# Kernel optimization log

Measured on AMD Instinct MI355X. Metric: run time of the kernel, lower is better.

The kernel has to match this reference:

```python
import jax, jax.numpy as jnp
import numpy as np

DIM = 32  # fixed internal node dim
N_GRAPHS = 64


def setup_inputs() -> dict:
    key = jax.random.key(0)
    ks = jax.random.split(key, 16)
    N, E, F_N, F_E, H = 12500, 200000, 16, 8, 32
    inp = {
        "x": jax.random.normal(ks[0], (N, F_N), dtype=jnp.float32),
        "edge_index": jax.random.randint(ks[1], (2, E), 0, N, dtype=jnp.int64),
        "edge_attr": jax.random.normal(ks[2], (E, F_E), dtype=jnp.float32),
        "batch": jnp.sort(jax.random.randint(ks[3], (N,), 0, N_GRAPHS, dtype=jnp.int64)),
        "lin0_w": jax.random.normal(ks[4], (DIM, F_N), dtype=jnp.float32) * 0.1,
        "lin0_b": jax.random.normal(ks[5], (DIM,), dtype=jnp.float32) * 0.1,
        "nn_w": jax.random.normal(ks[6], (DIM * H, F_E), dtype=jnp.float32) * 0.1,
        "nn_b": jax.random.normal(ks[7], (DIM * H,), dtype=jnp.float32) * 0.1,
        "root_w": jax.random.normal(ks[8], (DIM, H), dtype=jnp.float32) * 0.1,
        "conv_b": jax.random.normal(ks[9], (H,), dtype=jnp.float32) * 0.1,
        "lin1_w": jax.random.normal(ks[10], (16, H), dtype=jnp.float32) * 0.1,
        "lin1_b": jax.random.normal(ks[11], (16,), dtype=jnp.float32) * 0.1,
        "lin2_w": jax.random.normal(ks[12], (1, 16), dtype=jnp.float32) * 0.1,
        "lin2_b": jax.random.normal(ks[13], (1,), dtype=jnp.float32) * 0.1,
    }
    return inp


def reference(x, edge_index, edge_attr, batch, lin0_w, lin0_b, nn_w, nn_b,
              root_w, conv_b, lin1_w, lin1_b, lin2_w, lin2_b):
    N = x.shape[0]
    H = conv_b.shape[0]
    # lin0 + relu -> node features [N, DIM]
    out = jax.nn.relu(x @ lin0_w.T + lin0_b)
    # NNConv: per-edge weight matrices from edge MLP (single Linear)
    src, dst = edge_index[0], edge_index[1]
    w_e = (edge_attr @ nn_w.T + nn_b).reshape(-1, DIM, H)  # [E, DIM, H]
    msg = jnp.einsum('ed,edh->eh', out[src], w_e)          # gather + per-edge matmul
    agg = jax.ops.segment_sum(msg, dst, num_segments=N)     # scatter-add
    h = jax.nn.relu(agg + out @ root_w + conv_b)             # root weight + bias
    # global add pool over graphs
    u = jax.ops.segment_sum(h, batch, num_segments=N_GRAPHS)  # [G, H]
    o = jax.nn.relu(u @ lin1_w.T + lin1_b)
    o = o @ lin2_w.T + lin2_b
    return o.reshape(-1)
```

## Files before the change

kernel.cpp:

```cpp
#include <hip/hip_runtime.h>

#define DIMN 32
#define HD   32
#define FN   16
#define FE   8
#define NG   64

__global__ __launch_bounds__(256) void k1_node_pre(
    const float* __restrict__ x, const float* __restrict__ lin0_w,
    const float* __restrict__ lin0_b, const float* __restrict__ nn_w,
    const float* __restrict__ nn_b,
    float* __restrict__ outn, float* __restrict__ G, float* __restrict__ bmsg,
    int N, int nodes_per_block)
{
    __shared__ float s_nnw[DIMN * HD * FE];
    __shared__ float s_nnb[DIMN * HD];
    __shared__ float s_l0w[DIMN * FN];
    __shared__ float s_l0b[DIMN];
    __shared__ float s_out[DIMN];

    const int tid = threadIdx.x;
    for (int i = tid; i < DIMN * HD * FE; i += 256) s_nnw[i] = nn_w[i];
    for (int i = tid; i < DIMN * HD; i += 256)      s_nnb[i] = nn_b[i];
    for (int i = tid; i < DIMN * FN; i += 256)      s_l0w[i] = lin0_w[i];
    if (tid < DIMN) s_l0b[tid] = lin0_b[tid];
    __syncthreads();

    const int n0 = blockIdx.x * nodes_per_block;
    const int n1 = min(n0 + nodes_per_block, N);
    for (int n = n0; n < n1; ++n) {
        if (tid < DIMN) {
            float s = s_l0b[tid];
            const float* xr = x + (size_t)n * FN;
            #pragma unroll
            for (int j = 0; j < FN; ++j) s = fmaf(xr[j], s_l0w[tid * FN + j], s);
            s = fmaxf(s, 0.f);
            s_out[tid] = s;
            outn[(size_t)n * DIMN + tid] = s;
        }
        __syncthreads();

        float g = 0.f;
        #pragma unroll 8
        for (int d = 0; d < DIMN; ++d)
            g = fmaf(s_out[d], s_nnw[d * 256 + tid], g);
        G[(size_t)n * 256 + tid] = g;

        if (tid < HD) {
            float b = 0.f;
            #pragma unroll 8
            for (int d = 0; d < DIMN; ++d)
                b = fmaf(s_out[d], s_nnb[d * HD + tid], b);
            bmsg[(size_t)n * HD + tid] = b;
        }
        __syncthreads();
    }
}

__global__ __launch_bounds__(256) void k2_edge(
    const int* __restrict__ ei, const float* __restrict__ ea,
    const float* __restrict__ G, const float* __restrict__ bmsg,
    float* __restrict__ agg, int E)
{
    const int t = blockIdx.x * 256 + threadIdx.x;
    const int e = t >> 5;
    const int h = t & 31;
    if (e >= E) return;

    const int src = ei[e];
    const int dst = ei[E + e];

    const float* gp = G + (size_t)src * 256 + h * 8;
    const float4 ga = *(const float4*)(gp);
    const float4 gb = *(const float4*)(gp + 4);
    const float4 e0 = *(const float4*)(ea + (size_t)e * 8);
    const float4 e1 = *(const float4*)(ea + (size_t)e * 8 + 4);

    float acc = bmsg[(size_t)src * HD + h];
    acc = fmaf(e0.x, ga.x, acc);
    acc = fmaf(e0.y, ga.y, acc);
    acc = fmaf(e0.z, ga.z, acc);
    acc = fmaf(e0.w, ga.w, acc);
    acc = fmaf(e1.x, gb.x, acc);
    acc = fmaf(e1.y, gb.y, acc);
    acc = fmaf(e1.z, gb.z, acc);
    acc = fmaf(e1.w, gb.w, acc);

    atomicAdd(agg + (size_t)dst * HD + h, acc);
}

__global__ __launch_bounds__(256) void k3_node_upd(
    const float* __restrict__ agg, const float* __restrict__ outn,
    const float* __restrict__ root_w, const float* __restrict__ conv_b,
    const int* __restrict__ batch, float* __restrict__ u, int N)
{
    __shared__ float s_rw[DIMN * HD];
    __shared__ float s_cb[HD];
    const int tid = threadIdx.x;
    for (int i = tid; i < DIMN * HD; i += 256) s_rw[i] = root_w[i];
    if (tid < HD) s_cb[tid] = conv_b[tid];
    __syncthreads();

    const int t = blockIdx.x * 256 + tid;
    const int n = t >> 5;
    const int h = t & 31;
    if (n >= N) return;

    float v = agg[(size_t)n * HD + h] + s_cb[h];
    const float* orow = outn + (size_t)n * DIMN;
    #pragma unroll 8
    for (int k = 0; k < DIMN; ++k)
        v = fmaf(orow[k], s_rw[k * HD + h], v);
    v = fmaxf(v, 0.f);

    atomicAdd(u + (size_t)batch[n] * HD + h, v);
}

__global__ __launch_bounds__(64) void k4_head(
    const float* __restrict__ u, const float* __restrict__ lin1_w,
    const float* __restrict__ lin1_b, const float* __restrict__ lin2_w,
    const float* __restrict__ lin2_b, float* __restrict__ outp)
{
    const int g = threadIdx.x;
    if (g >= NG) return;

    float ur[HD];
    #pragma unroll
    for (int hh = 0; hh < HD; ++hh) ur[hh] = u[(size_t)g * HD + hh];

    float acc = lin2_b[0];
    #pragma unroll
    for (int i = 0; i < 16; ++i) {
        float o = lin1_b[i];
        #pragma unroll
        for (int hh = 0; hh < HD; ++hh)
            o = fmaf(ur[hh], lin1_w[i * HD + hh], o);
        o = fmaxf(o, 0.f);
        acc = fmaf(o, lin2_w[i], acc);
    }
    outp[g] = acc;
}

extern "C" void kernel_launch(void* const* d_in, const int* in_sizes, int n_in,
                              void* d_out, int out_size, void* d_ws, size_t ws_size,
                              hipStream_t stream)
{
    const float* x      = (const float*)d_in[0];
    const int*   ei     = (const int*)  d_in[1];
    const float* ea     = (const float*)d_in[2];
    const int*   batch  = (const int*)  d_in[3];
    const float* lin0_w = (const float*)d_in[4];
    const float* lin0_b = (const float*)d_in[5];
    const float* nn_w   = (const float*)d_in[6];
    const float* nn_b   = (const float*)d_in[7];
    const float* root_w = (const float*)d_in[8];
    const float* conv_b = (const float*)d_in[9];
    const float* lin1_w = (const float*)d_in[10];
    const float* lin1_b = (const float*)d_in[11];
    const float* lin2_w = (const float*)d_in[12];
    const float* lin2_b = (const float*)d_in[13];

    const int N = in_sizes[0] / FN;
    const int E = in_sizes[2] / FE;

    float* ws   = (float*)d_ws;
    float* outn = ws;
    float* G    = outn + (size_t)N * DIMN;
    float* bmsg = G    + (size_t)N * 256;
    float* agg  = bmsg + (size_t)N * DIMN;
    float* u    = agg  + (size_t)N * DIMN;

    hipMemsetAsync(agg, 0, (size_t)N * DIMN * sizeof(float), stream);
    hipMemsetAsync(u,   0, (size_t)NG * HD * sizeof(float), stream);

    const int npb = 16;
    const int nb1 = (N + npb - 1) / npb;
    k1_node_pre<<<nb1, 256, 0, stream>>>(x, lin0_w, lin0_b, nn_w, nn_b,
                                         outn, G, bmsg, N, npb);

    const int nb2 = (E * 32 + 255) / 256;
    k2_edge<<<nb2, 256, 0, stream>>>(ei, ea, G, bmsg, agg, E);

    const int nb3 = (N * 32 + 255) / 256;
    k3_node_upd<<<nb3, 256, 0, stream>>>(agg, outn, root_w, conv_b, batch, u, N);

    k4_head<<<1, 64, 0, stream>>>(u, lin1_w, lin1_b, lin2_w, lin2_b, (float*)d_out);
}
```

Measured before the change: 173.8 us.

## Replace atomic edge scatter with CSR-by-destination gather and segmented pooling

Builds a destination-sorted edge list each call (histogram, scan, scatter) and computes each node's aggregated message by pulling its incoming edges, fusing the root update and ReLU. Global pooling is replaced by a per-graph binary-search segment reduction fused with the MLP head. This removes millions of float atomics and the memsets. In exchange it adds three extra launches, a serial single-block scan, dependent indirect loads and load imbalance across nodes with varying in-degree.

```diff
diff --git a/kernel.cpp b/kernel.cpp
--- a/kernel.cpp
+++ b/kernel.cpp
@@ -11,6 +11,7 @@
     const float* __restrict__ lin0_b, const float* __restrict__ nn_w,
     const float* __restrict__ nn_b,
     float* __restrict__ outn, float* __restrict__ G, float* __restrict__ bmsg,
+    int* __restrict__ cnt,
     int N, int nodes_per_block)
 {
     __shared__ float s_nnw[DIMN * HD * FE];
@@ -20,6 +21,9 @@
     __shared__ float s_out[DIMN];
 
     const int tid = threadIdx.x;
+    const int gz = blockIdx.x * 256 + tid;
+    if (gz < N) cnt[gz] = 0;
+
     for (int i = tid; i < DIMN * HD * FE; i += 256) s_nnw[i] = nn_w[i];
     for (int i = tid; i < DIMN * HD; i += 256)      s_nnb[i] = nn_b[i];
     for (int i = tid; i < DIMN * FN; i += 256)      s_l0w[i] = lin0_w[i];
@@ -57,42 +61,56 @@
     }
 }
 
-__global__ __launch_bounds__(256) void k2_edge(
+__global__ __launch_bounds__(256) void k_hist(
+    const int* __restrict__ ei, int* __restrict__ cnt, int E)
+{
+    const int e = blockIdx.x * 256 + threadIdx.x;
+    if (e < E) atomicAdd(&cnt[ei[E + e]], 1);
+}
+
+__global__ __launch_bounds__(256) void k_scan(
+    const int* __restrict__ cnt, int* __restrict__ offs, int* __restrict__ cur, int N)
+{
+    __shared__ int s[256];
+    const int tid = threadIdx.x;
+    const int C = (N + 255) / 256;
+    const int lo = tid * C, hi = min(lo + C, N);
+    int sum = 0;
+    for (int i = lo; i < hi; ++i) sum += cnt[i];
+    s[tid] = sum;
+    __syncthreads();
+    for (int off = 1; off < 256; off <<= 1) {
+        int v = (tid >= off) ? s[tid - off] : 0;
+        __syncthreads();
+        s[tid] += v;
+        __syncthreads();
+    }
+    int run = (tid == 0) ? 0 : s[tid - 1];
+    for (int i = lo; i < hi; ++i) {
+        offs[i] = run;
+        cur[i]  = run;
+        run += cnt[i];
+    }
+    if (tid == 0) offs[N] = s[255];
+}
+
+__global__ __launch_bounds__(256) void k_scatter(
+    const int* __restrict__ ei, int* __restrict__ cur, int* __restrict__ eids, int E)
+{
+    const int e = blockIdx.x * 256 + threadIdx.x;
+    if (e < E) {
+        int p = atomicAdd(&cur[ei[E + e]], 1);
+        eids[p] = e;
+    }
+}
+
+__global__ __launch_bounds__(256) void k2_gather(
     const int* __restrict__ ei, const float* __restrict__ ea,
     const float* __restrict__ G, const float* __restrict__ bmsg,
-    float* __restrict__ agg, int E)
-{
-    const int t = blockIdx.x * 256 + threadIdx.x;
-    const int e = t >> 5;
-    const int h = t & 31;
-    if (e >= E) return;
-
-    const int src = ei[e];
-    const int dst = ei[E + e];
-
-    const float* gp = G + (size_t)src * 256 + h * 8;
-    const float4 ga = *(const float4*)(gp);
-    const float4 gb = *(const float4*)(gp + 4);
-    const float4 e0 = *(const float4*)(ea + (size_t)e * 8);
-    const float4 e1 = *(const float4*)(ea + (size_t)e * 8 + 4);
-
-    float acc = bmsg[(size_t)src * HD + h];
-    acc = fmaf(e0.x, ga.x, acc);
-    acc = fmaf(e0.y, ga.y, acc);
-    acc = fmaf(e0.z, ga.z, acc);
-    acc = fmaf(e0.w, ga.w, acc);
-    acc = fmaf(e1.x, gb.x, acc);
-    acc = fmaf(e1.y, gb.y, acc);
-    acc = fmaf(e1.z, gb.z, acc);
-    acc = fmaf(e1.w, gb.w, acc);
-
-    atomicAdd(agg + (size_t)dst * HD + h, acc);
-}
-
-__global__ __launch_bounds__(256) void k3_node_upd(
-    const float* __restrict__ agg, const float* __restrict__ outn,
-    const float* __restrict__ root_w, const float* __restrict__ conv_b,
-    const int* __restrict__ batch, float* __restrict__ u, int N)
+    const float* __restrict__ outn, const float* __restrict__ root_w,
+    const float* __restrict__ conv_b,
+    const int* __restrict__ offs, const int* __restrict__ eids,
+    float* __restrict__ hout, int N, int E)
 {
     __shared__ float s_rw[DIMN * HD];
     __shared__ float s_cb[HD];
@@ -106,39 +124,77 @@
     const int h = t & 31;
     if (n >= N) return;
 
-    float v = agg[(size_t)n * HD + h] + s_cb[h];
+    float acc = 0.f;
+    const int lo = offs[n], hi = offs[n + 1];
+    for (int j = lo; j < hi; ++j) {
+        const int e   = eids[j];
+        const int src = ei[e];
+        const float* gp = G + (size_t)src * 256 + h * 8;
+        const float4 ga = *(const float4*)(gp);
+        const float4 gb = *(const float4*)(gp + 4);
+        const float4 e0 = *(const float4*)(ea + (size_t)e * 8);
+        const float4 e1 = *(const float4*)(ea + (size_t)e * 8 + 4);
+        float m = bmsg[(size_t)src * HD + h];
+        m = fmaf(e0.x, ga.x, m);
+        m = fmaf(e0.y, ga.y, m);
+        m = fmaf(e0.z, ga.z, m);
+        m = fmaf(e0.w, ga.w, m);
+        m = fmaf(e1.x, gb.x, m);
+        m = fmaf(e1.y, gb.y, m);
+        m = fmaf(e1.z, gb.z, m);
+        m = fmaf(e1.w, gb.w, m);
+        acc += m;
+    }
+
+    float v = acc + s_cb[h];
     const float* orow = outn + (size_t)n * DIMN;
     #pragma unroll 8
     for (int k = 0; k < DIMN; ++k)
         v = fmaf(orow[k], s_rw[k * HD + h], v);
-    v = fmaxf(v, 0.f);
-
-    atomicAdd(u + (size_t)batch[n] * HD + h, v);
-}
-
-__global__ __launch_bounds__(64) void k4_head(
-    const float* __restrict__ u, const float* __restrict__ lin1_w,
-    const float* __restrict__ lin1_b, const float* __restrict__ lin2_w,
-    const float* __restrict__ lin2_b, float* __restrict__ outp)
-{
-    const int g = threadIdx.x;
-    if (g >= NG) return;
-
-    float ur[HD];
-    #pragma unroll
-    for (int hh = 0; hh < HD; ++hh) ur[hh] = u[(size_t)g * HD + hh];
-
-    float acc = lin2_b[0];
-    #pragma unroll
-    for (int i = 0; i < 16; ++i) {
-        float o = lin1_b[i];
+    hout[(size_t)n * HD + h] = fmaxf(v, 0.f);
+}
+
+__global__ __launch_bounds__(64) void k4_pool_head(
+    const float* __restrict__ hout, const int* __restrict__ batch,
+    const float* __restrict__ lin1_w, const float* __restrict__ lin1_b,
+    const float* __restrict__ lin2_w, const float* __restrict__ lin2_b,
+    float* __restrict__ outp, int N)
+{
+    const int g = blockIdx.x;
+    const int tid = threadIdx.x;
+
+    int a = 0, b = N;
+    while (a < b) { int m = (a + b) >> 1; if (batch[m] < g) a = m + 1; else b = m; }
+    const int lo = a;
+    b = N;
+    while (a < b) { int m = (a + b) >> 1; if (batch[m] < g + 1) a = m + 1; else b = m; }
+    const int hi = a;
+
+    __shared__ float s_u[HD];
+    __shared__ float s_o[16];
+
+    const int h = tid & 31, half = tid >> 5;
+    float s = 0.f;
+    for (int n = lo + half; n < hi; n += 2)
+        s += hout[(size_t)n * HD + h];
+    s += __shfl_down(s, 32);
+    if (tid < HD) s_u[tid] = s;
+    __syncthreads();
+
+    if (tid < 16) {
+        float o = lin1_b[tid];
         #pragma unroll
-        for (int hh = 0; hh < HD; ++hh)
-            o = fmaf(ur[hh], lin1_w[i * HD + hh], o);
-        o = fmaxf(o, 0.f);
-        acc = fmaf(o, lin2_w[i], acc);
-    }
-    outp[g] = acc;
+        for (int k = 0; k < HD; ++k) o = fmaf(s_u[k], lin1_w[tid * HD + k], o);
+        s_o[tid] = fmaxf(o, 0.f);
+    }
+    __syncthreads();
+
+    if (tid == 0) {
+        float acc = lin2_b[0];
+        #pragma unroll
+        for (int i = 0; i < 16; ++i) acc = fmaf(s_o[i], lin2_w[i], acc);
+        outp[g] = acc;
+    }
 }
 
 extern "C" void kernel_launch(void* const* d_in, const int* in_sizes, int n_in,
@@ -167,22 +223,26 @@
     float* outn = ws;
     float* G    = outn + (size_t)N * DIMN;
     float* bmsg = G    + (size_t)N * 256;
-    float* agg  = bmsg + (size_t)N * DIMN;
-    float* u    = agg  + (size_t)N * DIMN;
-
-    hipMemsetAsync(agg, 0, (size_t)N * DIMN * sizeof(float), stream);
-    hipMemsetAsync(u,   0, (size_t)NG * HD * sizeof(float), stream);
+    float* hout = bmsg + (size_t)N * DIMN;
+    int*   cnt  = (int*)(hout + (size_t)N * DIMN);
+    int*   offs = cnt  + N;
+    int*   cur  = offs + N + 1;
+    int*   eids = cur  + N;
 
     const int npb = 16;
     const int nb1 = (N + npb - 1) / npb;
     k1_node_pre<<<nb1, 256, 0, stream>>>(x, lin0_w, lin0_b, nn_w, nn_b,
-                                         outn, G, bmsg, N, npb);
-
-    const int nb2 = (E * 32 + 255) / 256;
-    k2_edge<<<nb2, 256, 0, stream>>>(ei, ea, G, bmsg, agg, E);
-
-    const int nb3 = (N * 32 + 255) / 256;
-    k3_node_upd<<<nb3, 256, 0, stream>>>(agg, outn, root_w, conv_b, batch, u, N);
-
-    k4_head<<<1, 64, 0, stream>>>(u, lin1_w, lin1_b, lin2_w, lin2_b, (float*)d_out);
-}
+                                         outn, G, bmsg, cnt, N, npb);
+
+    const int nbe = (E + 255) / 256;
+    k_hist<<<nbe, 256, 0, stream>>>(ei, cnt, E);
+    k_scan<<<1, 256, 0, stream>>>(cnt, offs, cur, N);
+    k_scatter<<<nbe, 256, 0, stream>>>(ei, cur, eids, E);
+
+    const int nb2 = (N * 32 + 255) / 256;
+    k2_gather<<<nb2, 256, 0, stream>>>(ei, ea, G, bmsg, outn, root_w, conv_b,
+                                       offs, eids, hout, N, E);
+
+    k4_pool_head<<<NG, 64, 0, stream>>>(hout, batch, lin1_w, lin1_b,
+                                        lin2_w, lin2_b, (float*)d_out, N);
+}
```

After: 236.2 us. 1.36x slower.

## Fuse edge, node-update and head into one cooperative kernel; batch node precompute

Applied to the files above, without the earlier changes.

Replaces the edge, node-update and head kernels with a single persistent cooperative kernel that uses grid-wide syncs between phases. The memsets are folded into the node-precompute kernel, which now processes 8 nodes at a time so each nn_w value read from shared memory is reused across those nodes. This removes several launches and memset calls and cuts shared-memory traffic in the precompute. The cost is two grid barriers, grid-stride loops over a capped block count, and occupancy-query host calls on every launch.

```diff
diff --git a/kernel.cpp b/kernel.cpp
--- a/kernel.cpp
+++ b/kernel.cpp
@@ -1,98 +1,97 @@
 #include <hip/hip_runtime.h>
+#include <hip/hip_cooperative_groups.h>
+
+namespace cg = cooperative_groups;
 
 #define DIMN 32
 #define HD   32
 #define FN   16
 #define FE   8
 #define NG   64
+#define MB   8
+#define NPB  32
 
 __global__ __launch_bounds__(256) void k1_node_pre(
     const float* __restrict__ x, const float* __restrict__ lin0_w,
     const float* __restrict__ lin0_b, const float* __restrict__ nn_w,
     const float* __restrict__ nn_b,
     float* __restrict__ outn, float* __restrict__ G, float* __restrict__ bmsg,
-    int N, int nodes_per_block)
+    float* __restrict__ agg, float* __restrict__ u, int N)
 {
     __shared__ float s_nnw[DIMN * HD * FE];
     __shared__ float s_nnb[DIMN * HD];
-    __shared__ float s_l0w[DIMN * FN];
+    __shared__ float s_l0wT[FN * DIMN];
     __shared__ float s_l0b[DIMN];
-    __shared__ float s_out[DIMN];
+    __shared__ float s_x[MB * FN];
+    __shared__ float s_out[MB * DIMN];
 
     const int tid = threadIdx.x;
+
+    for (int i = blockIdx.x * 256 + tid; i < N * HD; i += gridDim.x * 256)
+        agg[i] = 0.f;
+    if (blockIdx.x == 0)
+        for (int i = tid; i < NG * HD; i += 256) u[i] = 0.f;
+
     for (int i = tid; i < DIMN * HD * FE; i += 256) s_nnw[i] = nn_w[i];
     for (int i = tid; i < DIMN * HD; i += 256)      s_nnb[i] = nn_b[i];
-    for (int i = tid; i < DIMN * FN; i += 256)      s_l0w[i] = lin0_w[i];
+    for (int i = tid; i < FN * DIMN; i += 256)
+        s_l0wT[(i & 15) * DIMN + (i >> 4)] = lin0_w[i];
     if (tid < DIMN) s_l0b[tid] = lin0_b[tid];
     __syncthreads();
 
-    const int n0 = blockIdx.x * nodes_per_block;
-    const int n1 = min(n0 + nodes_per_block, N);
-    for (int n = n0; n < n1; ++n) {
-        if (tid < DIMN) {
-            float s = s_l0b[tid];
-            const float* xr = x + (size_t)n * FN;
+    const int n0 = blockIdx.x * NPB;
+    const int n1 = min(n0 + NPB, N);
+    const int m = tid >> 5, d = tid & 31;
+
+    for (int nb = n0; nb < n1; nb += MB) {
+        const int cnt = min(MB, n1 - nb);
+        if (tid < cnt * FN) s_x[tid] = x[(size_t)nb * FN + tid];
+        __syncthreads();
+
+        if (m < cnt) {
+            float s = s_l0b[d];
             #pragma unroll
-            for (int j = 0; j < FN; ++j) s = fmaf(xr[j], s_l0w[tid * FN + j], s);
+            for (int j = 0; j < FN; ++j)
+                s = fmaf(s_x[m * FN + j], s_l0wT[j * DIMN + d], s);
             s = fmaxf(s, 0.f);
-            s_out[tid] = s;
-            outn[(size_t)n * DIMN + tid] = s;
+            s_out[m * DIMN + d] = s;
+            outn[(size_t)(nb + m) * DIMN + d] = s;
         }
         __syncthreads();
 
-        float g = 0.f;
-        #pragma unroll 8
-        for (int d = 0; d < DIMN; ++d)
-            g = fmaf(s_out[d], s_nnw[d * 256 + tid], g);
-        G[(size_t)n * 256 + tid] = g;
-
-        if (tid < HD) {
+        float g[MB];
+        #pragma unroll
+        for (int mm = 0; mm < MB; ++mm) g[mm] = 0.f;
+        for (int dd = 0; dd < DIMN; ++dd) {
+            const float w = s_nnw[dd * 256 + tid];
+            #pragma unroll
+            for (int mm = 0; mm < MB; ++mm)
+                g[mm] = fmaf(s_out[mm * DIMN + dd], w, g[mm]);
+        }
+        #pragma unroll
+        for (int mm = 0; mm < MB; ++mm)
+            if (mm < cnt) G[(size_t)(nb + mm) * 256 + tid] = g[mm];
+
+        if (m < cnt) {
             float b = 0.f;
             #pragma unroll 8
-            for (int d = 0; d < DIMN; ++d)
-                b = fmaf(s_out[d], s_nnb[d * HD + tid], b);
-            bmsg[(size_t)n * HD + tid] = b;
+            for (int dd = 0; dd < DIMN; ++dd)
+                b = fmaf(s_out[m * DIMN + dd], s_nnb[dd * HD + d], b);
+            bmsg[(size_t)(nb + m) * HD + d] = b;
         }
         __syncthreads();
     }
 }
 
-__global__ __launch_bounds__(256) void k2_edge(
+__global__ __launch_bounds__(256, 8) void kcoop(
     const int* __restrict__ ei, const float* __restrict__ ea,
     const float* __restrict__ G, const float* __restrict__ bmsg,
-    float* __restrict__ agg, int E)
-{
-    const int t = blockIdx.x * 256 + threadIdx.x;
-    const int e = t >> 5;
-    const int h = t & 31;
-    if (e >= E) return;
-
-    const int src = ei[e];
-    const int dst = ei[E + e];
-
-    const float* gp = G + (size_t)src * 256 + h * 8;
-    const float4 ga = *(const float4*)(gp);
-    const float4 gb = *(const float4*)(gp + 4);
-    const float4 e0 = *(const float4*)(ea + (size_t)e * 8);
-    const float4 e1 = *(const float4*)(ea + (size_t)e * 8 + 4);
-
-    float acc = bmsg[(size_t)src * HD + h];
-    acc = fmaf(e0.x, ga.x, acc);
-    acc = fmaf(e0.y, ga.y, acc);
-    acc = fmaf(e0.z, ga.z, acc);
-    acc = fmaf(e0.w, ga.w, acc);
-    acc = fmaf(e1.x, gb.x, acc);
-    acc = fmaf(e1.y, gb.y, acc);
-    acc = fmaf(e1.z, gb.z, acc);
-    acc = fmaf(e1.w, gb.w, acc);
-
-    atomicAdd(agg + (size_t)dst * HD + h, acc);
-}
-
-__global__ __launch_bounds__(256) void k3_node_upd(
-    const float* __restrict__ agg, const float* __restrict__ outn,
-    const float* __restrict__ root_w, const float* __restrict__ conv_b,
-    const int* __restrict__ batch, float* __restrict__ u, int N)
+    const float* __restrict__ outn, const float* __restrict__ root_w,
+    const float* __restrict__ conv_b, const int* __restrict__ batch,
+    const float* __restrict__ lin1_w, const float* __restrict__ lin1_b,
+    const float* __restrict__ lin2_w, const float* __restrict__ lin2_b,
+    float* __restrict__ agg, float* __restrict__ u, float* __restrict__ outp,
+    int N, int E)
 {
     __shared__ float s_rw[DIMN * HD];
     __shared__ float s_cb[HD];
@@ -101,44 +100,63 @@
     if (tid < HD) s_cb[tid] = conv_b[tid];
     __syncthreads();
 
-    const int t = blockIdx.x * 256 + tid;
-    const int n = t >> 5;
-    const int h = t & 31;
-    if (n >= N) return;
-
-    float v = agg[(size_t)n * HD + h] + s_cb[h];
-    const float* orow = outn + (size_t)n * DIMN;
-    #pragma unroll 8
-    for (int k = 0; k < DIMN; ++k)
-        v = fmaf(orow[k], s_rw[k * HD + h], v);
-    v = fmaxf(v, 0.f);
-
-    atomicAdd(u + (size_t)batch[n] * HD + h, v);
-}
-
-__global__ __launch_bounds__(64) void k4_head(
-    const float* __restrict__ u, const float* __restrict__ lin1_w,
-    const float* __restrict__ lin1_b, const float* __restrict__ lin2_w,
-    const float* __restrict__ lin2_b, float* __restrict__ outp)
-{
-    const int g = threadIdx.x;
-    if (g >= NG) return;
-
-    float ur[HD];
-    #pragma unroll
-    for (int hh = 0; hh < HD; ++hh) ur[hh] = u[(size_t)g * HD + hh];
-
-    float acc = lin2_b[0];
-    #pragma unroll
-    for (int i = 0; i < 16; ++i) {
-        float o = lin1_b[i];
-        #pragma unroll
-        for (int hh = 0; hh < HD; ++hh)
-            o = fmaf(ur[hh], lin1_w[i * HD + hh], o);
-        o = fmaxf(o, 0.f);
-        acc = fmaf(o, lin2_w[i], acc);
-    }
-    outp[g] = acc;
+    const long stride = (long)gridDim.x * 256;
+
+    for (long t = (long)blockIdx.x * 256 + tid; t < (long)E * HD; t += stride) {
+        const int e = (int)(t >> 5);
+        const int h = (int)(t & 31);
+        const int src = ei[e];
+        const int dst = ei[E + e];
+        const float* gp = G + (size_t)src * 256 + h * 8;
+        const float4 ga = *(const float4*)(gp);
+        const float4 gb = *(const float4*)(gp + 4);
+        const float4 e0 = *(const float4*)(ea + (size_t)e * FE);
+        const float4 e1 = *(const float4*)(ea + (size_t)e * FE + 4);
+        float msg = bmsg[(size_t)src * HD + h];
+        msg = fmaf(e0.x, ga.x, msg);
+        msg = fmaf(e0.y, ga.y, msg);
+        msg = fmaf(e0.z, ga.z, msg);
+        msg = fmaf(e0.w, ga.w, msg);
+        msg = fmaf(e1.x, gb.x, msg);
+        msg = fmaf(e1.y, gb.y, msg);
+        msg = fmaf(e1.z, gb.z, msg);
+        msg = fmaf(e1.w, gb.w, msg);
+        atomicAdd(agg + (size_t)dst * HD + h, msg);
+    }
+
+    cg::this_grid().sync();
+
+    for (int t = blockIdx.x * 256 + tid; t < N * HD; t += (int)stride) {
+        const int n = t >> 5;
+        const int h = t & 31;
+        float v = agg[t] + s_cb[h];
+        const float* orow = outn + (size_t)n * DIMN;
+        #pragma unroll 8
+        for (int k = 0; k < DIMN; ++k)
+            v = fmaf(orow[k], s_rw[k * HD + h], v);
+        v = fmaxf(v, 0.f);
+        atomicAdd(u + (size_t)batch[n] * HD + h, v);
+    }
+
+    cg::this_grid().sync();
+
+    if (blockIdx.x == 0 && tid < NG) {
+        const int g = tid;
+        float ur[HD];
+        #pragma unroll
+        for (int hh = 0; hh < HD; ++hh) ur[hh] = u[(size_t)g * HD + hh];
+        float acc = lin2_b[0];
+        #pragma unroll
+        for (int i = 0; i < 16; ++i) {
+            float o = lin1_b[i];
+            #pragma unroll
+            for (int hh = 0; hh < HD; ++hh)
+                o = fmaf(ur[hh], lin1_w[i * HD + hh], o);
+            o = fmaxf(o, 0.f);
+            acc = fmaf(o, lin2_w[i], acc);
+        }
+        outp[g] = acc;
+    }
 }
 
 extern "C" void kernel_launch(void* const* d_in, const int* in_sizes, int n_in,
@@ -169,20 +187,28 @@
     float* bmsg = G    + (size_t)N * 256;
     float* agg  = bmsg + (size_t)N * DIMN;
     float* u    = agg  + (size_t)N * DIMN;
-
-    hipMemsetAsync(agg, 0, (size_t)N * DIMN * sizeof(float), stream);
-    hipMemsetAsync(u,   0, (size_t)NG * HD * sizeof(float), stream);
-
-    const int npb = 16;
-    const int nb1 = (N + npb - 1) / npb;
+    float* outp = (float*)d_out;
+
+    const int nb1 = (N + NPB - 1) / NPB;
     k1_node_pre<<<nb1, 256, 0, stream>>>(x, lin0_w, lin0_b, nn_w, nn_b,
-                                         outn, G, bmsg, N, npb);
-
-    const int nb2 = (E * 32 + 255) / 256;
-    k2_edge<<<nb2, 256, 0, stream>>>(ei, ea, G, bmsg, agg, E);
-
-    const int nb3 = (N * 32 + 255) / 256;
-    k3_node_upd<<<nb3, 256, 0, stream>>>(agg, outn, root_w, conv_b, batch, u, N);
-
-    k4_head<<<1, 64, 0, stream>>>(u, lin1_w, lin1_b, lin2_w, lin2_b, (float*)d_out);
+                                         outn, G, bmsg, agg, u, N);
+
+    int maxBlocksPerCU = 0;
+    hipOccupancyMaxActiveBlocksPerMultiprocessor(&maxBlocksPerCU,
+        reinterpret_cast<const void*>(kcoop), 256, 0);
+    if (maxBlocksPerCU < 1) maxBlocksPerCU = 1;
+    int nblk = maxBlocksPerCU * 256;
+    const long work = (long)E * HD / 256;
+    if ((long)nblk > work) nblk = (int)work;
+    if (nblk > 2048) nblk = 2048;
+
+    int Nl = N, El = E;
+    void* args[] = {
+        (void*)&ei, (void*)&ea, (void*)&G, (void*)&bmsg, (void*)&outn,
+        (void*)&root_w, (void*)&conv_b, (void*)&batch,
+        (void*)&lin1_w, (void*)&lin1_b, (void*)&lin2_w, (void*)&lin2_b,
+        (void*)&agg, (void*)&u, (void*)&outp, (void*)&Nl, (void*)&El
+    };
+    hipLaunchCooperativeKernel(reinterpret_cast<const void*>(kcoop),
+                               dim3(nblk), dim3(256), args, 0, stream);
 }
```

Result: slower. 438.4 us (+152.2%).
